# Optimization experiments

Measured on AMD Instinct MI355X. Metric: run time of the kernel, lower is better.

The kernel has to match this reference:

```python
import jax, jax.numpy as jnp
import numpy as np

B, S, D = 256, 512, 256
ATT = 128

def setup_inputs() -> dict:
    key = jax.random.key(0)
    k1, k2, k3, k4 = jax.random.split(key, 4)
    x = jax.random.normal(k1, (B, S, D), dtype=jnp.float32)
    W = jax.random.normal(k2, (D, ATT), dtype=jnp.float32)
    b = jax.random.normal(k3, (ATT,), dtype=jnp.float32)
    u = jax.random.normal(k4, (ATT, 1), dtype=jnp.float32)
    return {"x": x, "W": W, "b": b, "u": u}

def reference(x, W, b, u):
    # uit: [B, S, ATT]
    uit = jnp.tanh(jnp.einsum('bsd,da->bsa', x, W) + b)
    # scores: [B, S]  (faithful: exp without max-subtraction, as in original)
    ait = jnp.exp(jnp.einsum('bsa,a->bs', uit, u[:, 0]))
    ait = ait / (jnp.sum(ait, axis=1, keepdims=True) + 1e-08)
    # weighted sum over seq -> [B, D]
    return jnp.einsum('bsd,bs->bd', x, ait)
```

## Files before the change

### kernel.cpp

```cpp
#include <hip/hip_runtime.h>
#include <math.h>

typedef _Float16 f16x8 __attribute__((ext_vector_type(8)));
typedef float    f32x4 __attribute__((ext_vector_type(4)));

constexpr int B_ = 256, S_ = 512, D_ = 256, A_ = 128;

__device__ __forceinline__ float tanh_fast(float v) {
    return 1.0f - 2.0f / (1.0f + __expf(2.0f * v));
}

__global__ __launch_bounds__(512, 2) void k_fused(
    const float* __restrict__ x, const float* __restrict__ W,
    const float* __restrict__ bvec, const float* __restrict__ u,
    float* __restrict__ out)
{
    __shared__ _Float16 xh[16 * 64 * 8];
    __shared__ _Float16 xl[16 * 64 * 8];
    __shared__ float    part[2][8][32];
    __shared__ float    sc[S_];
    __shared__ float    red[8];
    __shared__ float    pbuf[8][D_];

    const int t    = threadIdx.x;
    const int lane = t & 63, wv = t >> 6;
    const int lr   = lane & 15, lg = lane >> 4;
    const int b    = blockIdx.x;
    const float* __restrict__ xb = x + (size_t)b * S_ * D_;

    f16x8 Bh[8], Bl[8];
#pragma unroll
    for (int ks = 0; ks < 8; ++ks) {
        const float* wp = W + (size_t)(ks * 32 + lg * 8) * A_ + wv * 16 + lr;
#pragma unroll
        for (int i = 0; i < 8; ++i) {
            float v = wp[(size_t)i * A_];
            _Float16 h = (_Float16)v;
            Bh[ks][i] = h;
            Bl[ks][i] = (_Float16)(v - (float)h);
        }
    }
    const float bb = bvec[wv * 16 + lr];
    const float uu = u[wv * 16 + lr];

    float4 ld[2][2];

#define K1_ISSUE(TT)                                                              \
    {                                                                             \
        _Pragma("unroll")                                                         \
        for (int ff = 0; ff < 2; ++ff) {                                          \
            int f = wv * 2 + ff;                                                  \
            const float* p = xb + (size_t)((TT) * 32 + ((f >> 3) << 4) + lr) * D_ \
                                + ((f & 7) << 5) + (lg << 3);                     \
            ld[ff][0] = *(const float4*)p;                                        \
            ld[ff][1] = *(const float4*)(p + 4);                                  \
        }                                                                         \
    }

#define K1_STAGE()                                                                \
    {                                                                             \
        _Pragma("unroll")                                                         \
        for (int ff = 0; ff < 2; ++ff) {                                          \
            int f = wv * 2 + ff;                                                  \
            float v[8] = {ld[ff][0].x, ld[ff][0].y, ld[ff][0].z, ld[ff][0].w,     \
                          ld[ff][1].x, ld[ff][1].y, ld[ff][1].z, ld[ff][1].w};    \
            f16x8 hi, lo;                                                         \
            _Pragma("unroll")                                                     \
            for (int i = 0; i < 8; ++i) {                                         \
                _Float16 h = (_Float16)v[i];                                      \
                hi[i] = h; lo[i] = (_Float16)(v[i] - (float)h);                   \
            }                                                                     \
            *(f16x8*)&xh[((size_t)f * 64 + lane) * 8] = hi;                       \
            *(f16x8*)&xl[((size_t)f * 64 + lane) * 8] = lo;                       \
        }                                                                         \
    }

    K1_ISSUE(0)
    K1_STAGE()

    for (int tt = 0; tt < 16; ++tt) {
        __syncthreads();
        if (tt > 0 && t < 32) {
            const float* pp = &part[(tt - 1) & 1][0][t];
            float ss = pp[0] + pp[32] + pp[64] + pp[96] + pp[128] + pp[160] + pp[192] + pp[224];
            sc[(tt - 1) * 32 + t] = __expf(ss);
        }
        if (tt < 15) K1_ISSUE(tt + 1)

        f32x4 acc0 = {0.f, 0.f, 0.f, 0.f}, acc1 = {0.f, 0.f, 0.f, 0.f};
#pragma unroll
        for (int ks = 0; ks < 8; ++ks) {
            f16x8 ah0 = *(const f16x8*)&xh[((size_t)(ks) * 64 + lane) * 8];
            f16x8 al0 = *(const f16x8*)&xl[((size_t)(ks) * 64 + lane) * 8];
            f16x8 ah1 = *(const f16x8*)&xh[((size_t)(8 + ks) * 64 + lane) * 8];
            f16x8 al1 = *(const f16x8*)&xl[((size_t)(8 + ks) * 64 + lane) * 8];
            acc0 = __builtin_amdgcn_mfma_f32_16x16x32_f16(ah0, Bh[ks], acc0, 0, 0, 0);
            acc0 = __builtin_amdgcn_mfma_f32_16x16x32_f16(ah0, Bl[ks], acc0, 0, 0, 0);
            acc0 = __builtin_amdgcn_mfma_f32_16x16x32_f16(al0, Bh[ks], acc0, 0, 0, 0);
            acc1 = __builtin_amdgcn_mfma_f32_16x16x32_f16(ah1, Bh[ks], acc1, 0, 0, 0);
            acc1 = __builtin_amdgcn_mfma_f32_16x16x32_f16(ah1, Bl[ks], acc1, 0, 0, 0);
            acc1 = __builtin_amdgcn_mfma_f32_16x16x32_f16(al1, Bh[ks], acc1, 0, 0, 0);
        }
#pragma unroll
        for (int mt = 0; mt < 2; ++mt) {
            f32x4 a = mt ? acc1 : acc0;
#pragma unroll
            for (int r = 0; r < 4; ++r) {
                float s = tanh_fast(a[r] + bb) * uu;
                s += __shfl_xor(s, 8, 64);
                s += __shfl_xor(s, 4, 64);
                s += __shfl_xor(s, 2, 64);
                s += __shfl_xor(s, 1, 64);
                if (lr == 0) part[tt & 1][wv][mt * 16 + lg * 4 + r] = s;
            }
        }
        __syncthreads();
        if (tt < 15) K1_STAGE()
    }
    if (t < 32) {
        const float* pp = &part[1][0][t];
        float ss = pp[0] + pp[32] + pp[64] + pp[96] + pp[128] + pp[160] + pp[192] + pp[224];
        sc[15 * 32 + t] = __expf(ss);
    }
    __syncthreads();
#undef K1_ISSUE
#undef K1_STAGE

    {
        float v = sc[wv * 64 + lane];
#pragma unroll
        for (int m = 32; m >= 1; m >>= 1) v += __shfl_xor(v, m, 64);
        if (lane == 0) red[wv] = v;
    }
    __syncthreads();
    float denom = 0.f;
#pragma unroll
    for (int i = 0; i < 8; ++i) denom += red[i];
    const float inv = 1.0f / (denom + 1e-8f);

    const float* xp = xb + (size_t)(wv * 64) * D_ + lane * 4;
    f32x4 a0 = {0.f, 0.f, 0.f, 0.f}, a1 = {0.f, 0.f, 0.f, 0.f};
#pragma unroll 8
    for (int j = 0; j < 64; j += 2) {
        float4 va = *(const float4*)(xp + (size_t)j * D_);
        float4 vb = *(const float4*)(xp + (size_t)(j + 1) * D_);
        float s0 = sc[wv * 64 + j], s1 = sc[wv * 64 + j + 1];
        a0[0] = fmaf(va.x, s0, a0[0]); a0[1] = fmaf(va.y, s0, a0[1]);
        a0[2] = fmaf(va.z, s0, a0[2]); a0[3] = fmaf(va.w, s0, a0[3]);
        a1[0] = fmaf(vb.x, s1, a1[0]); a1[1] = fmaf(vb.y, s1, a1[1]);
        a1[2] = fmaf(vb.z, s1, a1[2]); a1[3] = fmaf(vb.w, s1, a1[3]);
    }
    a0[0] += a1[0]; a0[1] += a1[1]; a0[2] += a1[2]; a0[3] += a1[3];
    *(f32x4*)&pbuf[wv][lane * 4] = a0;
    __syncthreads();

    if (t < D_) {
        float r = 0.f;
#pragma unroll
        for (int i = 0; i < 8; ++i) r += pbuf[i][t];
        out[b * D_ + t] = r * inv;
    }
}

extern "C" void kernel_launch(void* const* d_in, const int* in_sizes, int n_in,
                              void* d_out, int out_size, void* d_ws, size_t ws_size,
                              hipStream_t stream)
{
    const float* x    = (const float*)d_in[0];
    const float* W    = (const float*)d_in[1];
    const float* bvec = (const float*)d_in[2];
    const float* u    = (const float*)d_in[3];
    float* out = (float*)d_out;

    k_fused<<<B_, 512, 0, stream>>>(x, W, bvec, u, out);
}
```

Baseline: 217.4 us.

## Prepack W splits, double-buffer raw x tiles, retile waves over M/N halves

```diff
diff --git a/kernel.cpp b/kernel.cpp
--- a/kernel.cpp
+++ b/kernel.cpp
@@ -10,38 +10,58 @@
     return 1.0f - 2.0f / (1.0f + __expf(2.0f * v));
 }
 
+__global__ __launch_bounds__(256) void k_packW(const float* __restrict__ W,
+                                               _Float16* __restrict__ Wh,
+                                               _Float16* __restrict__ Wl)
+{
+    int tid = blockIdx.x * 256 + threadIdx.x;
+    int l  = tid & 63;
+    int nf = (tid >> 6) & 7;
+    int ks = tid >> 9;
+    int n  = nf * 16 + (l & 15);
+    int k0 = ks * 32 + ((l >> 4) & 3) * 8;
+    f16x8 hi, lo;
+#pragma unroll
+    for (int i = 0; i < 8; ++i) {
+        float v = W[(k0 + i) * A_ + n];
+        _Float16 h = (_Float16)v;
+        hi[i] = h;
+        lo[i] = (_Float16)(v - (float)h);
+    }
+    *(f16x8*)(Wh + (size_t)tid * 8) = hi;
+    *(f16x8*)(Wl + (size_t)tid * 8) = lo;
+}
+
 __global__ __launch_bounds__(512, 2) void k_fused(
-    const float* __restrict__ x, const float* __restrict__ W,
-    const float* __restrict__ bvec, const float* __restrict__ u,
-    float* __restrict__ out)
+    const float* __restrict__ x, const _Float16* __restrict__ Wh,
+    const _Float16* __restrict__ Wl, const float* __restrict__ bvec,
+    const float* __restrict__ u, float* __restrict__ out)
 {
-    __shared__ _Float16 xh[16 * 64 * 8];
-    __shared__ _Float16 xl[16 * 64 * 8];
-    __shared__ float    part[2][8][32];
-    __shared__ float    sc[S_];
-    __shared__ float    red[8];
-    __shared__ float    pbuf[8][D_];
+    __shared__ float xbuf[2][16][2][64][4];
+    __shared__ float sc[S_];
+    __shared__ float part[2][4][32];
+    __shared__ float red[8];
+    float* pbuf = &xbuf[0][0][0][0][0];
 
     const int t    = threadIdx.x;
     const int lane = t & 63, wv = t >> 6;
     const int lr   = lane & 15, lg = lane >> 4;
+    const int mth  = wv >> 2;
+    const int nfp  = wv & 3;
     const int b    = blockIdx.x;
     const float* __restrict__ xb = x + (size_t)b * S_ * D_;
 
-    f16x8 Bh[8], Bl[8];
+    f16x8 Bh[8][2], Bl[8][2];
 #pragma unroll
-    for (int ks = 0; ks < 8; ++ks) {
-        const float* wp = W + (size_t)(ks * 32 + lg * 8) * A_ + wv * 16 + lr;
+    for (int ks = 0; ks < 8; ++ks)
 #pragma unroll
-        for (int i = 0; i < 8; ++i) {
-            float v = wp[(size_t)i * A_];
-            _Float16 h = (_Float16)v;
-            Bh[ks][i] = h;
-            Bl[ks][i] = (_Float16)(v - (float)h);
+        for (int j = 0; j < 2; ++j) {
+            int nf = 2 * nfp + j;
+            Bh[ks][j] = *(const f16x8*)(Wh + ((size_t)(ks * 8 + nf) * 64 + lane) * 8);
+            Bl[ks][j] = *(const f16x8*)(Wl + ((size_t)(ks * 8 + nf) * 64 + lane) * 8);
         }
-    }
-    const float bb = bvec[wv * 16 + lr];
-    const float uu = u[wv * 16 + lr];
+    const float bb0 = bvec[(2 * nfp + 0) * 16 + lr], uu0 = u[(2 * nfp + 0) * 16 + lr];
+    const float bb1 = bvec[(2 * nfp + 1) * 16 + lr], uu1 = u[(2 * nfp + 1) * 16 + lr];
 
     float4 ld[2][2];
 
@@ -56,71 +76,64 @@
             ld[ff][1] = *(const float4*)(p + 4);                                  \
         }                                                                         \
     }
-
-#define K1_STAGE()                                                                \
+#define K1_STAGE(P)                                                               \
     {                                                                             \
         _Pragma("unroll")                                                         \
         for (int ff = 0; ff < 2; ++ff) {                                          \
             int f = wv * 2 + ff;                                                  \
-            float v[8] = {ld[ff][0].x, ld[ff][0].y, ld[ff][0].z, ld[ff][0].w,     \
-                          ld[ff][1].x, ld[ff][1].y, ld[ff][1].z, ld[ff][1].w};    \
-            f16x8 hi, lo;                                                         \
-            _Pragma("unroll")                                                     \
-            for (int i = 0; i < 8; ++i) {                                         \
-                _Float16 h = (_Float16)v[i];                                      \
-                hi[i] = h; lo[i] = (_Float16)(v[i] - (float)h);                   \
-            }                                                                     \
-            *(f16x8*)&xh[((size_t)f * 64 + lane) * 8] = hi;                       \
-            *(f16x8*)&xl[((size_t)f * 64 + lane) * 8] = lo;                       \
+            *(float4*)&xbuf[P][f][0][lane][0] = ld[ff][0];                        \
+            *(float4*)&xbuf[P][f][1][lane][0] = ld[ff][1];                        \
         }                                                                         \
     }
 
     K1_ISSUE(0)
-    K1_STAGE()
+    K1_STAGE(0)
 
     for (int tt = 0; tt < 16; ++tt) {
         __syncthreads();
         if (tt > 0 && t < 32) {
             const float* pp = &part[(tt - 1) & 1][0][t];
-            float ss = pp[0] + pp[32] + pp[64] + pp[96] + pp[128] + pp[160] + pp[192] + pp[224];
-            sc[(tt - 1) * 32 + t] = __expf(ss);
+            sc[(tt - 1) * 32 + t] = __expf(pp[0] + pp[32] + pp[64] + pp[96]);
         }
         if (tt < 15) K1_ISSUE(tt + 1)
 
+        const int p = tt & 1;
         f32x4 acc0 = {0.f, 0.f, 0.f, 0.f}, acc1 = {0.f, 0.f, 0.f, 0.f};
 #pragma unroll
         for (int ks = 0; ks < 8; ++ks) {
-            f16x8 ah0 = *(const f16x8*)&xh[((size_t)(ks) * 64 + lane) * 8];
-            f16x8 al0 = *(const f16x8*)&xl[((size_t)(ks) * 64 + lane) * 8];
-            f16x8 ah1 = *(const f16x8*)&xh[((size_t)(8 + ks) * 64 + lane) * 8];
-            f16x8 al1 = *(const f16x8*)&xl[((size_t)(8 + ks) * 64 + lane) * 8];
-            acc0 = __builtin_amdgcn_mfma_f32_16x16x32_f16(ah0, Bh[ks], acc0, 0, 0, 0);
-            acc0 = __builtin_amdgcn_mfma_f32_16x16x32_f16(ah0, Bl[ks], acc0, 0, 0, 0);
-            acc0 = __builtin_amdgcn_mfma_f32_16x16x32_f16(al0, Bh[ks], acc0, 0, 0, 0);
-            acc1 = __builtin_amdgcn_mfma_f32_16x16x32_f16(ah1, Bh[ks], acc1, 0, 0, 0);
-            acc1 = __builtin_amdgcn_mfma_f32_16x16x32_f16(ah1, Bl[ks], acc1, 0, 0, 0);
-            acc1 = __builtin_amdgcn_mfma_f32_16x16x32_f16(al1, Bh[ks], acc1, 0, 0, 0);
+            const int f = mth * 8 + ks;
+            f32x4 a0 = *(const f32x4*)&xbuf[p][f][0][lane][0];
+            f32x4 a1 = *(const f32x4*)&xbuf[p][f][1][lane][0];
+            f16x8 ah, al;
+#pragma unroll
+            for (int i = 0; i < 4; ++i) {
+                _Float16 h0 = (_Float16)a0[i];
+                _Float16 h1 = (_Float16)a1[i];
+                ah[i]     = h0; al[i]     = (_Float16)(a0[i] - (float)h0);
+                ah[4 + i] = h1; al[4 + i] = (_Float16)(a1[i] - (float)h1);
+            }
+            acc0 = __builtin_amdgcn_mfma_f32_16x16x32_f16(ah, Bh[ks][0], acc0, 0, 0, 0);
+            acc0 = __builtin_amdgcn_mfma_f32_16x16x32_f16(ah, Bl[ks][0], acc0, 0, 0, 0);
+            acc0 = __builtin_amdgcn_mfma_f32_16x16x32_f16(al, Bh[ks][0], acc0, 0, 0, 0);
+            acc1 = __builtin_amdgcn_mfma_f32_16x16x32_f16(ah, Bh[ks][1], acc1, 0, 0, 0);
+            acc1 = __builtin_amdgcn_mfma_f32_16x16x32_f16(ah, Bl[ks][1], acc1, 0, 0, 0);
+            acc1 = __builtin_amdgcn_mfma_f32_16x16x32_f16(al, Bh[ks][1], acc1, 0, 0, 0);
         }
 #pragma unroll
-        for (int mt = 0; mt < 2; ++mt) {
-            f32x4 a = mt ? acc1 : acc0;
-#pragma unroll
-            for (int r = 0; r < 4; ++r) {
-                float s = tanh_fast(a[r] + bb) * uu;
-                s += __shfl_xor(s, 8, 64);
-                s += __shfl_xor(s, 4, 64);
-                s += __shfl_xor(s, 2, 64);
-                s += __shfl_xor(s, 1, 64);
-                if (lr == 0) part[tt & 1][wv][mt * 16 + lg * 4 + r] = s;
-            }
+        for (int r = 0; r < 4; ++r) {
+            float s = tanh_fast(acc0[r] + bb0) * uu0 + tanh_fast(acc1[r] + bb1) * uu1;
+            s += __shfl_xor(s, 8, 64);
+            s += __shfl_xor(s, 4, 64);
+            s += __shfl_xor(s, 2, 64);
+            s += __shfl_xor(s, 1, 64);
+            if (lr == 0) part[tt & 1][nfp][mth * 16 + lg * 4 + r] = s;
         }
-        __syncthreads();
-        if (tt < 15) K1_STAGE()
+        if (tt < 15) K1_STAGE((tt + 1) & 1)
     }
+    __syncthreads();
     if (t < 32) {
         const float* pp = &part[1][0][t];
-        float ss = pp[0] + pp[32] + pp[64] + pp[96] + pp[128] + pp[160] + pp[192] + pp[224];
-        sc[15 * 32 + t] = __expf(ss);
+        sc[15 * 32 + t] = __expf(pp[0] + pp[32] + pp[64] + pp[96]);
     }
     __syncthreads();
 #undef K1_ISSUE
@@ -151,13 +164,13 @@
         a1[2] = fmaf(vb.z, s1, a1[2]); a1[3] = fmaf(vb.w, s1, a1[3]);
     }
     a0[0] += a1[0]; a0[1] += a1[1]; a0[2] += a1[2]; a0[3] += a1[3];
-    *(f32x4*)&pbuf[wv][lane * 4] = a0;
+    *(f32x4*)&pbuf[wv * 256 + lane * 4] = a0;
     __syncthreads();
 
     if (t < D_) {
         float r = 0.f;
 #pragma unroll
-        for (int i = 0; i < 8; ++i) r += pbuf[i][t];
+        for (int i = 0; i < 8; ++i) r += pbuf[i * 256 + t];
         out[b * D_ + t] = r * inv;
     }
 }
@@ -172,5 +185,9 @@
     const float* u    = (const float*)d_in[3];
     float* out = (float*)d_out;
 
-    k_fused<<<B_, 512, 0, stream>>>(x, W, bvec, u, out);
+    _Float16* Wh = (_Float16*)d_ws;
+    _Float16* Wl = (_Float16*)((char*)d_ws + 65536);
+
+    k_packW<<<16, 256, 0, stream>>>(W, Wh, Wl);
+    k_fused<<<B_, 512, 0, stream>>>(x, Wh, Wl, bvec, u, out);
 }
```

New measurement: 240.8 us. 1.11x slower.
